# Performance work log

Measured on AMD Instinct MI355X. Metric: run time of the kernel, lower is better.

The kernel has to match this reference:

```python
import jax, jax.numpy as jnp
import numpy as np

D_MODEL = 1024
NHEAD = 16


def setup_inputs() -> dict:
    key = jax.random.key(0)
    ks = jax.random.split(key, 11)
    B, S, D = 4, 2048, D_MODEL
    scale = 1.0 / np.sqrt(D)
    inp = {
        "q": jax.random.normal(ks[0], (B, S, D), jnp.float32),
        "k": jax.random.normal(ks[1], (B, S, D), jnp.float32),
        "v": jax.random.normal(ks[2], (B, S, D), jnp.float32),
        "Wq": jax.random.normal(ks[3], (D, D), jnp.float32) * scale,
        "bq": jnp.zeros((D,), jnp.float32),
        "Wk": jax.random.normal(ks[4], (D, D), jnp.float32) * scale,
        "bk": jnp.zeros((D,), jnp.float32),
        "Wv": jax.random.normal(ks[5], (D, D), jnp.float32) * scale,
        "bv": jnp.zeros((D,), jnp.float32),
        "Wo": jax.random.normal(ks[6], (D, D), jnp.float32) * scale,
        "bo": jnp.zeros((D,), jnp.float32),
    }
    return inp


def reference(q, k, v, Wq, bq, Wk, bk, Wv, bv, Wo, bo):
    # Linear projections (torch Linear: x @ W.T + b)
    qp = jnp.einsum("bsd,ed->bse", q, Wq) + bq
    kp = jnp.einsum("bsd,ed->bse", k, Wk) + bk
    vp = jnp.einsum("bsd,ed->bse", v, Wv) + bv
    # NOTE: no head split; full-width attention with per-head scale
    scale = 1.0 / np.sqrt(D_MODEL / NHEAD)  # sqrt(d_model/nhead)
    scores = jnp.einsum("bqd,bkd->bqk", qp, kp) * scale  # [B,S,S]
    attn = jax.nn.softmax(scores, axis=-1)
    out = jnp.einsum("bqk,bkd->bqd", attn, vp)
    return jnp.einsum("bsd,ed->bse", out, Wo) + bo
```

## Files before the change

### kernel.cpp

```cpp
#include <hip/hip_runtime.h>
#include <hip/hip_fp16.h>

typedef __attribute__((ext_vector_type(8))) _Float16 half8;
typedef __attribute__((ext_vector_type(4))) float floatx4;
typedef __attribute__((ext_vector_type(8))) ushort ushortx8;

#define TILE 128
#define BK 32

__device__ inline ushort f2h(float f) {
    _Float16 h = (_Float16)f;
    ushort u; __builtin_memcpy(&u, &h, 2); return u;
}
__device__ inline float h2f(ushort u) {
    _Float16 h; __builtin_memcpy(&h, &u, 2);
    return (float)h;
}

__device__ inline void async_copy16(const ushort* g, ushort* lds) {
    __builtin_amdgcn_global_load_lds(
        (const __attribute__((address_space(1))) void*)(const void*)g,
        (__attribute__((address_space(3))) void*)(void*)lds,
        16, 0, 0);
}

template<int OM, bool TRANS, bool HB>
__global__ __launch_bounds__(256)
void gemm_nt(const ushort* __restrict__ A, long long batchA, int lda,
             const ushort* __restrict__ B, long long batchB, int ldb,
             void* __restrict__ C, long long batchC, int ldc,
             const float* __restrict__ bias, float scale, int K)
{
    __shared__ ushort As[TILE * 32];
    __shared__ ushort Bs[TILE * 32];

    const int bz    = blockIdx.z;
    const int tileM = blockIdx.y * TILE;
    const int tileN = blockIdx.x * TILE;
    const ushort* Ab = A + (size_t)bz * batchA + (size_t)tileM * lda;
    const ushort* Bb = B + (size_t)bz * batchB + (size_t)tileN * ldb;

    const int t    = threadIdx.x;
    const int lane = t & 63;
    const int wave = t >> 6;
    const int wr   = (wave >> 1) * 64;
    const int wc   = (wave & 1) * 64;
    const int lrow = lane & 15;

    const int srow = lane >> 2;
    const int scol = ((lane & 3) ^ ((lane >> 3) & 3)) * 8;
    const int chunk_sw = (((lane >> 4) ^ ((lane >> 1) & 3))) * 8;

    floatx4 acc[4][4];
#pragma unroll
    for (int i = 0; i < 4; i++)
#pragma unroll
        for (int j = 0; j < 4; j++) acc[i][j] = (floatx4){0.f, 0.f, 0.f, 0.f};

    for (int k0 = 0; k0 < K; k0 += BK) {
#pragma unroll
        for (int h = 0; h < 2; h++) {
            const int r0 = wave * 32 + h * 16;
            async_copy16(Ab + (size_t)(r0 + srow) * lda + k0 + scol, &As[r0 * 32]);
            async_copy16(Bb + (size_t)(r0 + srow) * ldb + k0 + scol, &Bs[r0 * 32]);
        }
        __syncthreads();

        half8 aF[4], bF[4];
#pragma unroll
        for (int i = 0; i < 4; i++) {
            aF[i] = *(const half8*)(&As[(wr + i * 16 + lrow) * 32 + chunk_sw]);
            bF[i] = *(const half8*)(&Bs[(wc + i * 16 + lrow) * 32 + chunk_sw]);
        }
#pragma unroll
        for (int i = 0; i < 4; i++)
#pragma unroll
            for (int j = 0; j < 4; j++)
                acc[i][j] = __builtin_amdgcn_mfma_f32_16x16x32_f16(aF[i], bF[j], acc[i][j], 0, 0, 0);
        __syncthreads();
    }

    const int rq = (lane >> 4) * 4;
#pragma unroll
    for (int i = 0; i < 4; i++) {
#pragma unroll
        for (int j = 0; j < 4; j++) {
            const int gn = tileN + wc + j * 16 + lrow;
            const float bv = HB ? bias[gn] : 0.f;
#pragma unroll
            for (int r = 0; r < 4; r++) {
                const int gm = tileM + wr + i * 16 + rq + r;
                const float val = acc[i][j][r] * scale + bv;
                const size_t idx = TRANS ? ((size_t)gn * ldc + gm) : ((size_t)gm * ldc + gn);
                if (OM == 0) {
                    float* Cf = (float*)C + (size_t)bz * batchC;
                    Cf[idx] = val;
                } else {
                    ushort* Ch = (ushort*)C + (size_t)bz * batchC;
                    Ch[idx] = f2h(val);
                }
            }
        }
    }
}

__global__ __launch_bounds__(256)
void cvt_f32_to_f16(const float* __restrict__ src, ushort* __restrict__ dst, int n)
{
    const int i = (blockIdx.x * 256 + threadIdx.x) * 8;
    if (i >= n) return;
    floatx4 f0 = *(const floatx4*)(src + i);
    floatx4 f1 = *(const floatx4*)(src + i + 4);
    ushortx8 u;
    u[0] = f2h(f0.x); u[1] = f2h(f0.y); u[2] = f2h(f0.z); u[3] = f2h(f0.w);
    u[4] = f2h(f1.x); u[5] = f2h(f1.y); u[6] = f2h(f1.z); u[7] = f2h(f1.w);
    *(ushortx8*)(dst + i) = u;
}

__global__ __launch_bounds__(256)
void softmax_rows(ushort* __restrict__ scores)
{
    const int S = 2048;
    ushort* srow = scores + (size_t)blockIdx.x * S;
    const int t    = threadIdx.x;
    const int lane = t & 63;
    const int w    = t >> 6;

    ushortx8 raw = *(const ushortx8*)(srow + t * 8);
    float l[8];
#pragma unroll
    for (int i = 0; i < 8; i++) l[i] = h2f(raw[i]);

    float m = l[0];
#pragma unroll
    for (int i = 1; i < 8; i++) m = fmaxf(m, l[i]);
#pragma unroll
    for (int off = 32; off >= 1; off >>= 1) m = fmaxf(m, __shfl_down(m, off));

    __shared__ float redm[4], reds[4];
    if (lane == 0) redm[w] = m;
    __syncthreads();
    m = fmaxf(fmaxf(redm[0], redm[1]), fmaxf(redm[2], redm[3]));

    float e[8], s = 0.f;
#pragma unroll
    for (int i = 0; i < 8; i++) { e[i] = __expf(l[i] - m); s += e[i]; }
#pragma unroll
    for (int off = 32; off >= 1; off >>= 1) s += __shfl_down(s, off);
    if (lane == 0) reds[w] = s;
    __syncthreads();
    s = reds[0] + reds[1] + reds[2] + reds[3];
    const float inv = 1.f / s;

    ushortx8 o;
#pragma unroll
    for (int i = 0; i < 8; i++) o[i] = f2h(e[i] * inv);
    *(ushortx8*)(srow + t * 8) = o;
}

extern "C" void kernel_launch(void* const* d_in, const int* in_sizes, int n_in,
                              void* d_out, int out_size, void* d_ws, size_t ws_size,
                              hipStream_t stream)
{
    const int B = 4, S = 2048, D = 1024;
    const size_t SD = (size_t)B * S * D;
    const float* q  = (const float*)d_in[0];
    const float* k  = (const float*)d_in[1];
    const float* v  = (const float*)d_in[2];
    const float* Wq = (const float*)d_in[3];
    const float* bq = (const float*)d_in[4];
    const float* Wk = (const float*)d_in[5];
    const float* bk = (const float*)d_in[6];
    const float* Wv = (const float*)d_in[7];
    const float* bv = (const float*)d_in[8];
    const float* Wo = (const float*)d_in[9];
    const float* bo = (const float*)d_in[10];
    float* out = (float*)d_out;

    ushort* q16  = (ushort*)d_ws;
    ushort* k16  = q16 + SD;
    ushort* qp   = k16 + SD;
    ushort* kp   = qp  + SD;
    ushort* sc   = kp  + SD;
    ushort* Wq16 = sc  + (size_t)B * S * S;
    ushort* Wk16 = Wq16 + (size_t)D * D;
    ushort* Wv16 = Wk16 + (size_t)D * D;
    ushort* Wo16 = Wv16 + (size_t)D * D;
    ushort* v16  = sc;
    ushort* vpt  = q16;
    ushort* attn = k16;

    dim3 blk(256);
    cvt_f32_to_f16<<<dim3((int)(SD / 2048)), blk, 0, stream>>>(q, q16, (int)SD);
    cvt_f32_to_f16<<<dim3((int)(SD / 2048)), blk, 0, stream>>>(k, k16, (int)SD);
    cvt_f32_to_f16<<<dim3((int)(SD / 2048)), blk, 0, stream>>>(v, v16, (int)SD);
    cvt_f32_to_f16<<<dim3(D * D / 2048), blk, 0, stream>>>(Wq, Wq16, D * D);
    cvt_f32_to_f16<<<dim3(D * D / 2048), blk, 0, stream>>>(Wk, Wk16, D * D);
    cvt_f32_to_f16<<<dim3(D * D / 2048), blk, 0, stream>>>(Wv, Wv16, D * D);
    cvt_f32_to_f16<<<dim3(D * D / 2048), blk, 0, stream>>>(Wo, Wo16, D * D);

    gemm_nt<1, false, true><<<dim3(D / TILE, (B * S) / TILE, 1), blk, 0, stream>>>(
        q16, 0, D, Wq16, 0, D, qp, 0, D, bq, 1.0f, D);
    gemm_nt<1, false, true><<<dim3(D / TILE, (B * S) / TILE, 1), blk, 0, stream>>>(
        k16, 0, D, Wk16, 0, D, kp, 0, D, bk, 1.0f, D);
    gemm_nt<1, true, true><<<dim3(D / TILE, S / TILE, B), blk, 0, stream>>>(
        v16, (long long)S * D, D, Wv16, 0, D, vpt, (long long)D * S, S, bv, 1.0f, D);
    gemm_nt<1, false, false><<<dim3(S / TILE, S / TILE, B), blk, 0, stream>>>(
        qp, (long long)S * D, D, kp, (long long)S * D, D,
        sc, (long long)S * S, S, nullptr, 0.125f, D);
    softmax_rows<<<dim3(B * S), blk, 0, stream>>>(sc);
    gemm_nt<1, false, false><<<dim3(D / TILE, S / TILE, B), blk, 0, stream>>>(
        sc, (long long)S * S, S, vpt, (long long)D * S, S,
        attn, (long long)S * D, D, nullptr, 1.0f, S);
    gemm_nt<0, false, true><<<dim3(D / TILE, (B * S) / TILE, 1), blk, 0, stream>>>(
        attn, 0, D, Wo16, 0, D, out, 0, D, bo, 1.0f, D);
}
```

Baseline: 428.2 us.

## Fuse input fp16 conversion into merged QKV projection kernel and double BK

Activation conversion from fp32 to fp16 now happens inside the GEMM load path, and the three Q/K/V projections run in a single launch, so the three separate conversion kernels and their fp16 intermediate buffers are gone. The four weight conversions are batched into one launch. BK grows from 32 to 64 with a new XOR swizzle, halving barrier count per K, at the cost of doubled LDS per block. The fp32 A-path uses synchronous register loads rather than async LDS copies, which may expose load latency in the projection GEMMs.

```diff
diff --git a/kernel.cpp b/kernel.cpp
--- a/kernel.cpp
+++ b/kernel.cpp
@@ -6,7 +6,7 @@
 typedef __attribute__((ext_vector_type(8))) ushort ushortx8;
 
 #define TILE 128
-#define BK 32
+#define BK 64
 
 __device__ inline ushort f2h(float f) {
     _Float16 h = (_Float16)f;
@@ -24,91 +24,169 @@
         16, 0, 0);
 }
 
-template<int OM, bool TRANS, bool HB>
-__global__ __launch_bounds__(256)
-void gemm_nt(const ushort* __restrict__ A, long long batchA, int lda,
-             const ushort* __restrict__ B, long long batchB, int ldb,
-             void* __restrict__ C, long long batchC, int ldc,
-             const float* __restrict__ bias, float scale, int K)
-{
-    __shared__ ushort As[TILE * 32];
-    __shared__ ushort Bs[TILE * 32];
-
-    const int bz    = blockIdx.z;
-    const int tileM = blockIdx.y * TILE;
-    const int tileN = blockIdx.x * TILE;
-    const ushort* Ab = A + (size_t)bz * batchA + (size_t)tileM * lda;
-    const ushort* Bb = B + (size_t)bz * batchB + (size_t)tileN * ldb;
-
+template<bool A_F32>
+__device__ __forceinline__ void gemm_core(const void* __restrict__ A, int lda,
+                                          const ushort* __restrict__ B, int ldb,
+                                          int K, ushort* As, ushort* Bs,
+                                          floatx4 acc[4][4])
+{
     const int t    = threadIdx.x;
     const int lane = t & 63;
     const int wave = t >> 6;
     const int wr   = (wave >> 1) * 64;
     const int wc   = (wave & 1) * 64;
     const int lrow = lane & 15;
-
-    const int srow = lane >> 2;
-    const int scol = ((lane & 3) ^ ((lane >> 3) & 3)) * 8;
-    const int chunk_sw = (((lane >> 4) ^ ((lane >> 1) & 3))) * 8;
-
-    floatx4 acc[4][4];
-#pragma unroll
-    for (int i = 0; i < 4; i++)
-#pragma unroll
-        for (int j = 0; j < 4; j++) acc[i][j] = (floatx4){0.f, 0.f, 0.f, 0.f};
+    const int srow = lane >> 3;
+    const int gcol = ((lane & 7) ^ srow) * 8;
+    const int c0   = lane >> 4;
+    const int sw   = lane & 7;
 
     for (int k0 = 0; k0 < K; k0 += BK) {
 #pragma unroll
-        for (int h = 0; h < 2; h++) {
-            const int r0 = wave * 32 + h * 16;
-            async_copy16(Ab + (size_t)(r0 + srow) * lda + k0 + scol, &As[r0 * 32]);
-            async_copy16(Bb + (size_t)(r0 + srow) * ldb + k0 + scol, &Bs[r0 * 32]);
+        for (int h = 0; h < 4; h++) {
+            const int r0 = wave * 32 + h * 8;
+            if (A_F32) {
+                const float* src = (const float*)A + (size_t)(r0 + srow) * lda + k0 + gcol;
+                floatx4 f0 = *(const floatx4*)src, f1 = *(const floatx4*)(src + 4);
+                ushortx8 u;
+                u[0] = f2h(f0.x); u[1] = f2h(f0.y); u[2] = f2h(f0.z); u[3] = f2h(f0.w);
+                u[4] = f2h(f1.x); u[5] = f2h(f1.y); u[6] = f2h(f1.z); u[7] = f2h(f1.w);
+                *(ushortx8*)(&As[(r0 + srow) * 64 + (lane & 7) * 8]) = u;
+            } else {
+                async_copy16((const ushort*)A + (size_t)(r0 + srow) * lda + k0 + gcol,
+                             &As[r0 * 64]);
+            }
+            async_copy16(B + (size_t)(r0 + srow) * ldb + k0 + gcol, &Bs[r0 * 64]);
         }
         __syncthreads();
 
-        half8 aF[4], bF[4];
-#pragma unroll
-        for (int i = 0; i < 4; i++) {
-            aF[i] = *(const half8*)(&As[(wr + i * 16 + lrow) * 32 + chunk_sw]);
-            bF[i] = *(const half8*)(&Bs[(wc + i * 16 + lrow) * 32 + chunk_sw]);
+#pragma unroll
+        for (int step = 0; step < 2; step++) {
+            half8 aF[4], bF[4];
+            const int ch = ((4 * step + c0) ^ sw) * 8;
+#pragma unroll
+            for (int i = 0; i < 4; i++) {
+                aF[i] = *(const half8*)(&As[(wr + i * 16 + lrow) * 64 + ch]);
+                bF[i] = *(const half8*)(&Bs[(wc + i * 16 + lrow) * 64 + ch]);
+            }
+#pragma unroll
+            for (int i = 0; i < 4; i++)
+#pragma unroll
+                for (int j = 0; j < 4; j++)
+                    acc[i][j] = __builtin_amdgcn_mfma_f32_16x16x32_f16(aF[i], bF[j], acc[i][j], 0, 0, 0);
         }
-#pragma unroll
-        for (int i = 0; i < 4; i++)
-#pragma unroll
-            for (int j = 0; j < 4; j++)
-                acc[i][j] = __builtin_amdgcn_mfma_f32_16x16x32_f16(aF[i], bF[j], acc[i][j], 0, 0, 0);
         __syncthreads();
     }
-
-    const int rq = (lane >> 4) * 4;
+}
+
+template<int OM, bool TRANS, bool HB>
+__device__ __forceinline__ void epilogue(floatx4 acc[4][4], void* Cb, int ldc,
+                                         const float* bias, float scale)
+{
+    const int lane = threadIdx.x & 63;
+    const int wave = threadIdx.x >> 6;
+    const int wr = (wave >> 1) * 64, wc = (wave & 1) * 64;
+    const int lrow = lane & 15, rq = (lane >> 4) * 4;
 #pragma unroll
     for (int i = 0; i < 4; i++) {
 #pragma unroll
         for (int j = 0; j < 4; j++) {
-            const int gn = tileN + wc + j * 16 + lrow;
-            const float bv = HB ? bias[gn] : 0.f;
+            const int n = wc + j * 16 + lrow;
+            const float bv = HB ? bias[n] : 0.f;
 #pragma unroll
             for (int r = 0; r < 4; r++) {
-                const int gm = tileM + wr + i * 16 + rq + r;
+                const int m = wr + i * 16 + rq + r;
                 const float val = acc[i][j][r] * scale + bv;
-                const size_t idx = TRANS ? ((size_t)gn * ldc + gm) : ((size_t)gm * ldc + gn);
-                if (OM == 0) {
-                    float* Cf = (float*)C + (size_t)bz * batchC;
-                    Cf[idx] = val;
-                } else {
-                    ushort* Ch = (ushort*)C + (size_t)bz * batchC;
-                    Ch[idx] = f2h(val);
-                }
+                const size_t idx = TRANS ? ((size_t)n * ldc + m) : ((size_t)m * ldc + n);
+                if (OM == 0) ((float*)Cb)[idx] = val;
+                else         ((ushort*)Cb)[idx] = f2h(val);
             }
         }
     }
 }
 
-__global__ __launch_bounds__(256)
-void cvt_f32_to_f16(const float* __restrict__ src, ushort* __restrict__ dst, int n)
-{
-    const int i = (blockIdx.x * 256 + threadIdx.x) * 8;
-    if (i >= n) return;
+template<int OM, bool TRANS, bool HB>
+__global__ __launch_bounds__(256)
+void gemm_nt(const ushort* __restrict__ A, long long batchA, int lda,
+             const ushort* __restrict__ B, long long batchB, int ldb,
+             void* __restrict__ C, long long batchC, int ldc,
+             const float* __restrict__ bias, float scale, int K)
+{
+    __shared__ ushort As[TILE * BK];
+    __shared__ ushort Bs[TILE * BK];
+    const int bz = blockIdx.z;
+    const int tileM = blockIdx.y * TILE, tileN = blockIdx.x * TILE;
+
+    floatx4 acc[4][4];
+#pragma unroll
+    for (int i = 0; i < 4; i++)
+#pragma unroll
+        for (int j = 0; j < 4; j++) acc[i][j] = (floatx4){0.f, 0.f, 0.f, 0.f};
+
+    gemm_core<false>(A + (size_t)bz * batchA + (size_t)tileM * lda, lda,
+                     B + (size_t)bz * batchB + (size_t)tileN * ldb, ldb,
+                     K, As, Bs, acc);
+
+    const size_t coff = TRANS ? ((size_t)tileN * ldc + tileM) : ((size_t)tileM * ldc + tileN);
+    void* Cb = (OM == 0) ? (void*)((float*)C + (size_t)bz * batchC + coff)
+                         : (void*)((ushort*)C + (size_t)bz * batchC + coff);
+    epilogue<OM, TRANS, HB>(acc, Cb, ldc, HB ? bias + tileN : nullptr, scale);
+}
+
+__global__ __launch_bounds__(256)
+void qkv_proj(const float* __restrict__ q, const float* __restrict__ k,
+              const float* __restrict__ v,
+              const ushort* __restrict__ Wq, const ushort* __restrict__ Wk,
+              const ushort* __restrict__ Wv,
+              const float* __restrict__ bq, const float* __restrict__ bk,
+              const float* __restrict__ bv,
+              ushort* __restrict__ qp, ushort* __restrict__ kp,
+              ushort* __restrict__ vpt)
+{
+    __shared__ ushort As[TILE * BK];
+    __shared__ ushort Bs[TILE * BK];
+    const int D = 1024, S = 2048;
+    const int y = blockIdx.y;
+    const int tileN = blockIdx.x * TILE;
+
+    floatx4 acc[4][4];
+#pragma unroll
+    for (int i = 0; i < 4; i++)
+#pragma unroll
+        for (int j = 0; j < 4; j++) acc[i][j] = (floatx4){0.f, 0.f, 0.f, 0.f};
+
+    if (y < 128) {
+        const bool isQ = (y < 64);
+        const int my = isQ ? y : y - 64;
+        const float* A  = (isQ ? q : k) + (size_t)my * TILE * D;
+        const ushort* W = (isQ ? Wq : Wk) + (size_t)tileN * D;
+        gemm_core<true>(A, D, W, D, D, As, Bs, acc);
+        ushort* Cb = (isQ ? qp : kp) + (size_t)my * TILE * D + tileN;
+        epilogue<1, false, true>(acc, Cb, D, (isQ ? bq : bk) + tileN, 1.0f);
+    } else {
+        const int yy = y - 128;
+        const int bz = yy >> 4, my = yy & 15;
+        const float* A = v + ((size_t)bz * S + (size_t)my * TILE) * D;
+        gemm_core<true>(A, D, Wv + (size_t)tileN * D, D, D, As, Bs, acc);
+        ushort* Cb = vpt + (size_t)bz * D * S + (size_t)tileN * S + (size_t)my * TILE;
+        epilogue<1, true, true>(acc, Cb, S, bv + tileN, 1.0f);
+    }
+}
+
+__global__ __launch_bounds__(256)
+void cvt_w(const float* __restrict__ w0, const float* __restrict__ w1,
+           const float* __restrict__ w2, const float* __restrict__ w3,
+           ushort* __restrict__ o0, ushort* __restrict__ o1,
+           ushort* __restrict__ o2, ushort* __restrict__ o3)
+{
+    const float* src; ushort* dst;
+    switch (blockIdx.y) {
+        case 0: src = w0; dst = o0; break;
+        case 1: src = w1; dst = o1; break;
+        case 2: src = w2; dst = o2; break;
+        default: src = w3; dst = o3; break;
+    }
+    const size_t i = ((size_t)blockIdx.x * 256 + threadIdx.x) * 8;
     floatx4 f0 = *(const floatx4*)(src + i);
     floatx4 f1 = *(const floatx4*)(src + i + 4);
     ushortx8 u;
@@ -177,41 +255,33 @@
     const float* bo = (const float*)d_in[10];
     float* out = (float*)d_out;
 
-    ushort* q16  = (ushort*)d_ws;
-    ushort* k16  = q16 + SD;
-    ushort* qp   = k16 + SD;
-    ushort* kp   = qp  + SD;
-    ushort* sc   = kp  + SD;
-    ushort* Wq16 = sc  + (size_t)B * S * S;
+    ushort* qp   = (ushort*)d_ws;
+    ushort* kp   = qp + SD;
+    ushort* sc   = kp + SD;
+    ushort* Wq16 = sc + (size_t)B * S * S;
     ushort* Wk16 = Wq16 + (size_t)D * D;
     ushort* Wv16 = Wk16 + (size_t)D * D;
     ushort* Wo16 = Wv16 + (size_t)D * D;
-    ushort* v16  = sc;
-    ushort* vpt  = q16;
-    ushort* attn = k16;
+    ushort* vpt  = Wo16 + (size_t)D * D;
+    ushort* attn = vpt + SD;
 
     dim3 blk(256);
-    cvt_f32_to_f16<<<dim3((int)(SD / 2048)), blk, 0, stream>>>(q, q16, (int)SD);
-    cvt_f32_to_f16<<<dim3((int)(SD / 2048)), blk, 0, stream>>>(k, k16, (int)SD);
-    cvt_f32_to_f16<<<dim3((int)(SD / 2048)), blk, 0, stream>>>(v, v16, (int)SD);
-    cvt_f32_to_f16<<<dim3(D * D / 2048), blk, 0, stream>>>(Wq, Wq16, D * D);
-    cvt_f32_to_f16<<<dim3(D * D / 2048), blk, 0, stream>>>(Wk, Wk16, D * D);
-    cvt_f32_to_f16<<<dim3(D * D / 2048), blk, 0, stream>>>(Wv, Wv16, D * D);
-    cvt_f32_to_f16<<<dim3(D * D / 2048), blk, 0, stream>>>(Wo, Wo16, D * D);
-
-    gemm_nt<1, false, true><<<dim3(D / TILE, (B * S) / TILE, 1), blk, 0, stream>>>(
-        q16, 0, D, Wq16, 0, D, qp, 0, D, bq, 1.0f, D);
-    gemm_nt<1, false, true><<<dim3(D / TILE, (B * S) / TILE, 1), blk, 0, stream>>>(
-        k16, 0, D, Wk16, 0, D, kp, 0, D, bk, 1.0f, D);
-    gemm_nt<1, true, true><<<dim3(D / TILE, S / TILE, B), blk, 0, stream>>>(
-        v16, (long long)S * D, D, Wv16, 0, D, vpt, (long long)D * S, S, bv, 1.0f, D);
+
+    cvt_w<<<dim3(D * D / 2048, 4), blk, 0, stream>>>(Wq, Wk, Wv, Wo, Wq16, Wk16, Wv16, Wo16);
+
+    qkv_proj<<<dim3(D / TILE, 192), blk, 0, stream>>>(
+        q, k, v, Wq16, Wk16, Wv16, bq, bk, bv, qp, kp, vpt);
+
     gemm_nt<1, false, false><<<dim3(S / TILE, S / TILE, B), blk, 0, stream>>>(
         qp, (long long)S * D, D, kp, (long long)S * D, D,
         sc, (long long)S * S, S, nullptr, 0.125f, D);
+
     softmax_rows<<<dim3(B * S), blk, 0, stream>>>(sc);
+
     gemm_nt<1, false, false><<<dim3(D / TILE, S / TILE, B), blk, 0, stream>>>(
         sc, (long long)S * S, S, vpt, (long long)D * S, S,
         attn, (long long)S * D, D, nullptr, 1.0f, S);
+
     gemm_nt<0, false, true><<<dim3(D / TILE, (B * S) / TILE, 1), blk, 0, stream>>>(
         attn, 0, D, Wo16, 0, D, out, 0, D, bo, 1.0f, D);
 }
```

Measured after the change: 384.4 us. 10.2% less time.
